# Performance work log

Hardware: AMD Instinct MI355X
Metric: run time of the kernel (lower is better)

The kernel has to match this reference:

```python
import jax, jax.numpy as jnp
import numpy as np

# Config: PointPillars KITTI-style BEV grid
BEV_H = 496
BEV_W = 432
B = 4          # batch size
C = 64         # pillar feature channels
M_PER = 30000  # non-empty pillars per sample


def setup_inputs() -> dict:
    key = jax.random.key(0)
    k_feat, k_coord = jax.random.split(key)
    voxel_features = jax.random.normal(k_feat, (B * M_PER, C), dtype=jnp.float32)
    # Collision-free coords per batch: sample M_PER unique cells from the H*W grid
    coords_list = []
    for b in range(B):
        perm = jax.random.permutation(jax.random.fold_in(k_coord, b), BEV_H * BEV_W)[:M_PER]
        y = (perm // BEV_W).astype(jnp.int32)
        x = (perm % BEV_W).astype(jnp.int32)
        bcol = jnp.full((M_PER,), b, dtype=jnp.int32)
        coords_list.append(jnp.stack([bcol, y, x], axis=1))
    voxel_coords = jnp.concatenate(coords_list, axis=0)  # (M, 3)
    return {"voxel_coords": voxel_coords, "voxel_features": voxel_features, "batch_size": B}


def reference(voxel_coords, voxel_features, batch_size):
    # voxel_coords: (M, 3) [batch_idx, y_idx, x_idx]; voxel_features: (M, C)
    c = voxel_features.shape[1]
    bi = voxel_coords[:, 0].astype(jnp.int32)
    yi = voxel_coords[:, 1].astype(jnp.int32)
    xi = voxel_coords[:, 2].astype(jnp.int32)
    flat = (bi * BEV_H + yi) * BEV_W + xi  # (M,) flat (b, y, x) index
    bev = jnp.zeros((batch_size * BEV_H * BEV_W, c), dtype=voxel_features.dtype)
    bev = bev.at[flat].set(voxel_features)  # single fused scatter over all batches
    # (B*H*W, C) -> (B, C, H, W)
    return bev.reshape(batch_size, BEV_H, BEV_W, c).transpose(0, 3, 1, 2)
```

## Files before the change

kernel.cpp:

```cpp
#include <hip/hip_runtime.h>


#define BEV_H 496
#define BEV_W 432
#define BB 4
#define CC 64
#define HW (BEV_H * BEV_W)
#define NQUAD (BB * HW / 4)
#define QBLOCKS (NQUAD / 256)

__global__ __launch_bounds__(256) void scatter_idx_kernel(
    const int* __restrict__ coords, int* __restrict__ map, int M) {
  int m = blockIdx.x * 256 + threadIdx.x;
  if (m >= M) return;
  int b = coords[3 * m + 0];
  int y = coords[3 * m + 1];
  int x = coords[3 * m + 2];
  map[(b * BEV_H + y) * BEV_W + x] = m;
}

__global__ __launch_bounds__(256) void gather4_kernel(
    const int4* __restrict__ map4, const float4* __restrict__ feat4,
    float4* __restrict__ out4) {
  int q = blockIdx.x * 256 + threadIdx.x;
  int cell = q * 4;
  int b = cell / HW;
  int hw0 = cell - b * HW;

  int4 mi = map4[q];
  int m0 = mi.x, m1 = mi.y, m2 = mi.z, m3 = mi.w;
  bool e0 = m0 < 0, e1 = m1 < 0, e2 = m2 < 0, e3 = m3 < 0;
  const float4* r0 = feat4 + (size_t)(e0 ? 0 : m0) * (CC / 4);
  const float4* r1 = feat4 + (size_t)(e1 ? 0 : m1) * (CC / 4);
  const float4* r2 = feat4 + (size_t)(e2 ? 0 : m2) * (CC / 4);
  const float4* r3 = feat4 + (size_t)(e3 ? 0 : m3) * (CC / 4);

  size_t obase = (size_t)b * CC * (HW / 4) + (hw0 >> 2);

#pragma unroll
  for (int c4 = 0; c4 < CC / 4; ++c4) {
    float4 a0 = r0[c4];
    float4 a1 = r1[c4];
    float4 a2 = r2[c4];
    float4 a3 = r3[c4];
    if (e0) a0 = make_float4(0.f, 0.f, 0.f, 0.f);
    if (e1) a1 = make_float4(0.f, 0.f, 0.f, 0.f);
    if (e2) a2 = make_float4(0.f, 0.f, 0.f, 0.f);
    if (e3) a3 = make_float4(0.f, 0.f, 0.f, 0.f);
    out4[obase + (size_t)(4 * c4 + 0) * (HW / 4)] = make_float4(a0.x, a1.x, a2.x, a3.x);
    out4[obase + (size_t)(4 * c4 + 1) * (HW / 4)] = make_float4(a0.y, a1.y, a2.y, a3.y);
    out4[obase + (size_t)(4 * c4 + 2) * (HW / 4)] = make_float4(a0.z, a1.z, a2.z, a3.z);
    out4[obase + (size_t)(4 * c4 + 3) * (HW / 4)] = make_float4(a0.w, a1.w, a2.w, a3.w);
  }
}

extern "C" void kernel_launch(void* const* d_in, const int* in_sizes, int n_in,
                              void* d_out, int out_size, void* d_ws, size_t ws_size,
                              hipStream_t stream) {
  const int*   coords = (const int*)d_in[0];
  const float* feat   = (const float*)d_in[1];
  float*       out    = (float*)d_out;
  int M = in_sizes[0] / 3;

  int* map = (int*)d_ws;

  hipMemsetAsync(map, 0xFF, (size_t)BB * HW * sizeof(int), stream);

  scatter_idx_kernel<<<(M + 255) / 256, 256, 0, stream>>>(coords, map, M);

  gather4_kernel<<<QBLOCKS, 256, 0, stream>>>(
      (const int4*)map, (const float4*)feat, (float4*)out);
}
```

Before: 260.8 us.

## Split gather work across channels per thread with shared-memory index staging

The gather kernel changes from one thread handling four cells across all 64 channels to a block of 256 threads handling 64 cells. Each thread now covers one float4 channel group for four cells. The 64 map indices are staged in shared memory, and feature reads from a pillar row are spread across threads. This gives more blocks and less per-thread serial work, at the cost of a __syncthreads and sixteen times more blocks.

```diff
diff --git a/kernel.cpp b/kernel.cpp
--- a/kernel.cpp
+++ b/kernel.cpp
@@ -6,8 +6,8 @@
 #define BB 4
 #define CC 64
 #define HW (BEV_H * BEV_W)
-#define NQUAD (BB * HW / 4)
-#define QBLOCKS (NQUAD / 256)
+#define CELLS_PER_BLOCK 64
+#define NBLOCKS (BB * HW / CELLS_PER_BLOCK)
 
 __global__ __launch_bounds__(256) void scatter_idx_kernel(
     const int* __restrict__ coords, int* __restrict__ map, int M) {
@@ -19,39 +19,39 @@
   map[(b * BEV_H + y) * BEV_W + x] = m;
 }
 
-__global__ __launch_bounds__(256) void gather4_kernel(
-    const int4* __restrict__ map4, const float4* __restrict__ feat4,
+__global__ __launch_bounds__(256) void gather_kernel(
+    const int* __restrict__ map, const float4* __restrict__ feat4,
     float4* __restrict__ out4) {
-  int q = blockIdx.x * 256 + threadIdx.x;
-  int cell = q * 4;
-  int b = cell / HW;
-  int hw0 = cell - b * HW;
+  __shared__ int smap[CELLS_PER_BLOCK];
+  const int cellbase = blockIdx.x * CELLS_PER_BLOCK;
+  const int tid = threadIdx.x;
 
-  int4 mi = map4[q];
-  int m0 = mi.x, m1 = mi.y, m2 = mi.z, m3 = mi.w;
-  bool e0 = m0 < 0, e1 = m1 < 0, e2 = m2 < 0, e3 = m3 < 0;
-  const float4* r0 = feat4 + (size_t)(e0 ? 0 : m0) * (CC / 4);
-  const float4* r1 = feat4 + (size_t)(e1 ? 0 : m1) * (CC / 4);
-  const float4* r2 = feat4 + (size_t)(e2 ? 0 : m2) * (CC / 4);
-  const float4* r3 = feat4 + (size_t)(e3 ? 0 : m3) * (CC / 4);
+  if (tid < CELLS_PER_BLOCK) smap[tid] = map[cellbase + tid];
+  __syncthreads();
 
-  size_t obase = (size_t)b * CC * (HW / 4) + (hw0 >> 2);
+  const int c4 = tid >> 4;
+  const int q  = tid & 15;
 
-#pragma unroll
-  for (int c4 = 0; c4 < CC / 4; ++c4) {
-    float4 a0 = r0[c4];
-    float4 a1 = r1[c4];
-    float4 a2 = r2[c4];
-    float4 a3 = r3[c4];
-    if (e0) a0 = make_float4(0.f, 0.f, 0.f, 0.f);
-    if (e1) a1 = make_float4(0.f, 0.f, 0.f, 0.f);
-    if (e2) a2 = make_float4(0.f, 0.f, 0.f, 0.f);
-    if (e3) a3 = make_float4(0.f, 0.f, 0.f, 0.f);
-    out4[obase + (size_t)(4 * c4 + 0) * (HW / 4)] = make_float4(a0.x, a1.x, a2.x, a3.x);
-    out4[obase + (size_t)(4 * c4 + 1) * (HW / 4)] = make_float4(a0.y, a1.y, a2.y, a3.y);
-    out4[obase + (size_t)(4 * c4 + 2) * (HW / 4)] = make_float4(a0.z, a1.z, a2.z, a3.z);
-    out4[obase + (size_t)(4 * c4 + 3) * (HW / 4)] = make_float4(a0.w, a1.w, a2.w, a3.w);
-  }
+  const int m0 = smap[4 * q + 0];
+  const int m1 = smap[4 * q + 1];
+  const int m2 = smap[4 * q + 2];
+  const int m3 = smap[4 * q + 3];
+
+  const float4 z = make_float4(0.f, 0.f, 0.f, 0.f);
+  float4 a0 = (m0 < 0) ? z : feat4[(size_t)m0 * (CC / 4) + c4];
+  float4 a1 = (m1 < 0) ? z : feat4[(size_t)m1 * (CC / 4) + c4];
+  float4 a2 = (m2 < 0) ? z : feat4[(size_t)m2 * (CC / 4) + c4];
+  float4 a3 = (m3 < 0) ? z : feat4[(size_t)m3 * (CC / 4) + c4];
+
+  const int b = cellbase / HW;
+  const int hwq = (cellbase - b * HW) >> 2;
+  const size_t obase =
+      (size_t)b * CC * (HW / 4) + (size_t)hwq + q + (size_t)(4 * c4) * (HW / 4);
+
+  out4[obase + 0 * (size_t)(HW / 4)] = make_float4(a0.x, a1.x, a2.x, a3.x);
+  out4[obase + 1 * (size_t)(HW / 4)] = make_float4(a0.y, a1.y, a2.y, a3.y);
+  out4[obase + 2 * (size_t)(HW / 4)] = make_float4(a0.z, a1.z, a2.z, a3.z);
+  out4[obase + 3 * (size_t)(HW / 4)] = make_float4(a0.w, a1.w, a2.w, a3.w);
 }
 
 extern "C" void kernel_launch(void* const* d_in, const int* in_sizes, int n_in,
@@ -68,6 +68,6 @@
 
   scatter_idx_kernel<<<(M + 255) / 256, 256, 0, stream>>>(coords, map, M);
 
-  gather4_kernel<<<QBLOCKS, 256, 0, stream>>>(
-      (const int4*)map, (const float4*)feat, (float4*)out);
+  gather_kernel<<<NBLOCKS, 256, 0, stream>>>(
+      map, (const float4*)feat, (float4*)out);
 }
```

Result: no change. 264.4 us (+1.4%).
